# Kernel tuning notes

Measured on AMD Instinct MI355X. Metric: run time of the kernel, lower is better.

## Reference

```python
import jax, jax.numpy as jnp
import numpy as np

NUM_HEADS = 4


def setup_inputs() -> dict:
    key = jax.random.key(0)
    ks = jax.random.split(key, 5)
    B, C, L = 8, 128, 2048
    x = jax.random.normal(ks[0], (B, C, L), dtype=jnp.float32)
    # Conv1d(C, 3C, 1) == per-position linear; weight [3C, C], bias [3C]
    w_qkv = jax.random.normal(ks[1], (3 * C, C), dtype=jnp.float32) * (1.0 / np.sqrt(C))
    b_qkv = jax.random.normal(ks[2], (3 * C,), dtype=jnp.float32) * 0.01
    w_proj = jax.random.normal(ks[3], (C, C), dtype=jnp.float32) * (1.0 / np.sqrt(C))
    b_proj = jax.random.normal(ks[4], (C,), dtype=jnp.float32) * 0.01
    return {"x": x, "w_qkv": w_qkv, "b_qkv": b_qkv, "w_proj": w_proj, "b_proj": b_proj}


def reference(x, w_qkv, b_qkv, w_proj, b_proj):
    B, C, L = x.shape
    H = NUM_HEADS
    D = C // H
    scale = D ** -0.5
    # 1x1 conv qkv projection: [B, 3C, L]
    qkv = jnp.einsum('oc,bcl->bol', w_qkv, x) + b_qkv[None, :, None]
    # reshape (B,3,H,D,L) -> permute to (3,B,H,L,D)
    qkv = qkv.reshape(B, 3, H, D, L).transpose(1, 0, 2, 4, 3)
    q, k, v = qkv[0], qkv[1], qkv[2]  # each [B, H, L, D]
    attn = jax.nn.softmax(jnp.einsum('bhld,bhmd->bhlm', q, k) * scale, axis=-1)
    out = jnp.einsum('bhlm,bhmd->bhld', attn, v)  # [B, H, L, D]
    out = out.transpose(0, 1, 3, 2).reshape(B, C, L)
    out = jnp.einsum('oc,bcl->bol', w_proj, out) + b_proj[None, :, None]
    return out + x
```

## Files before the change

### kernel.cpp

```cpp
#include <hip/hip_runtime.h>

#define Bsz 8
#define Cdim 128
#define Lseq 2048
#define NH 4
#define HD 32
#define BH 32
#define QSCALE (0.17677669529663687f * 1.4426950408889634f)

typedef __bf16 bf16x8 __attribute__((ext_vector_type(8)));
typedef float f32x4 __attribute__((ext_vector_type(4)));
typedef unsigned u32x4 __attribute__((ext_vector_type(4)));

__device__ __forceinline__ float fexp2(float x) {
#if __has_builtin(__builtin_amdgcn_exp2f)
    return __builtin_amdgcn_exp2f(x);
#else
    return __expf(x * 0.6931471805599453f);
#endif
}

__device__ __forceinline__ unsigned short f2bf(float f) {
    unsigned u = __builtin_bit_cast(unsigned, f);
    u += 0x7FFFu + ((u >> 16) & 1u);
    return (unsigned short)(u >> 16);
}

__device__ __forceinline__ unsigned pack_bf16(float a, float b) {
    return (unsigned)f2bf(a) | ((unsigned)f2bf(b) << 16);
}

__device__ __forceinline__ unsigned pack_bf16_rtz(float a, float b) {
    return __builtin_amdgcn_perm(__builtin_bit_cast(unsigned, b),
                                 __builtin_bit_cast(unsigned, a), 0x07060302u);
}

__device__ __forceinline__ float bf_lo(unsigned u) {
    return __builtin_bit_cast(float, u << 16);
}
__device__ __forceinline__ float bf_hi(unsigned u) {
    return __builtin_bit_cast(float, u & 0xFFFF0000u);
}

#define MFMA16(A, B, C) __builtin_amdgcn_mfma_f32_16x16x32_bf16((A), (B), (C), 0, 0, 0)

__global__ __launch_bounds__(256) void qkv_kernel(const float* __restrict__ x,
        const float* __restrict__ w, const float* __restrict__ bias,
        unsigned short* __restrict__ qh, unsigned short* __restrict__ kh,
        unsigned short* __restrict__ vh) {
    __shared__ __attribute__((aligned(16))) unsigned short T[64][132];
    int bid = blockIdx.x;
    int xcd = bid & 7;
    int s   = bid >> 3;
    int og3 = s % 3;
    int u_  = s / 3;
    int trio = u_ * 8 + xcd;
    int lt  = trio & 31;
    int b   = trio >> 5;
    int l0 = lt * 64;
    int t = threadIdx.x;
    int lane = t & 63, wv = t >> 6;
    int m16 = lane & 15, quad = lane >> 4;

    bf16x8 af[2][4];
    float bs[2][4];
    #pragma unroll
    for (int os = 0; os < 2; os++) {
        int orow = og3 * 128 + os * 64 + wv * 16;
        #pragma unroll
        for (int ks = 0; ks < 4; ks++) {
            const float* p = w + (size_t)(orow + m16) * Cdim + ks * 32 + quad * 8;
            float4 f0 = *(const float4*)p;
            float4 f1 = *(const float4*)(p + 4);
            u32x4 u = {pack_bf16(f0.x, f0.y), pack_bf16(f0.z, f0.w),
                       pack_bf16(f1.x, f1.y), pack_bf16(f1.z, f1.w)};
            af[os][ks] = __builtin_bit_cast(bf16x8, u);
        }
        #pragma unroll
        for (int r = 0; r < 4; r++) bs[os][r] = bias[orow + quad * 4 + r];
    }

    {
        int ll = t & 63, cg = t >> 6;
        const float* xb = x + (size_t)b * Cdim * Lseq + l0 + ll;
        #pragma unroll
        for (int i = 0; i < 16; i++) {
            int c = cg * 32 + 2 * i;
            float f0 = xb[(size_t)c * Lseq];
            float f1 = xb[(size_t)(c + 1) * Lseq];
            *(unsigned*)&T[ll][c] = pack_bf16(f0, f1);
        }
    }
    __syncthreads();

    #pragma unroll
    for (int ns = 0; ns < 4; ns++) {
        bf16x8 bx[4];
        #pragma unroll
        for (int ks = 0; ks < 4; ks++)
            bx[ks] = *(const bf16x8*)(&T[ns * 16 + m16][ks * 32 + quad * 8]);
        int l = l0 + ns * 16 + m16;
        #pragma unroll
        for (int os = 0; os < 2; os++) {
            f32x4 acc = {0.f, 0.f, 0.f, 0.f};
            #pragma unroll
            for (int ks = 0; ks < 4; ks++) acc = MFMA16(af[os][ks], bx[ks], acc);
            int oq = os * 64 + wv * 16 + quad * 4;
            if (og3 == 0) {
                int h = oq >> 5, d0 = oq & 31;
                uint2 u;
                u.x = pack_bf16((acc[0] + bs[os][0]) * QSCALE, (acc[1] + bs[os][1]) * QSCALE);
                u.y = pack_bf16((acc[2] + bs[os][2]) * QSCALE, (acc[3] + bs[os][3]) * QSCALE);
                *(uint2*)(qh + ((size_t)(b * NH + h) * Lseq + l) * HD + d0) = u;
            } else if (og3 == 1) {
                int h = oq >> 5, d0 = oq & 31;
                uint2 u;
                u.x = pack_bf16(acc[0] + bs[os][0], acc[1] + bs[os][1]);
                u.y = pack_bf16(acc[2] + bs[os][2], acc[3] + bs[os][3]);
                *(uint2*)(kh + ((size_t)(b * NH + h) * Lseq + l) * HD + d0) = u;
            } else {
                int kc = l >> 6, kk = l & 63;
                int half = kk >> 5, k32 = kk & 31;
                int q_, j_;
                if (k32 < 16) { q_ = k32 >> 2; j_ = k32 & 3; }
                else          { q_ = (k32 - 16) >> 2; j_ = 4 + ((k32 - 16) & 3); }
                int pos = half * 32 + q_ * 8 + j_;
                #pragma unroll
                for (int r = 0; r < 4; r++) {
                    int o = oq + r, h = o >> 5, d = o & 31;
                    vh[(((size_t)(b * NH + h) * 32 + kc) * HD + d) * 64 + pos] =
                        f2bf(acc[r] + bs[os][r]);
                }
            }
        }
    }
}

__global__ __launch_bounds__(256, 2) void attn_kernel(
        const unsigned short* __restrict__ qh, const unsigned short* __restrict__ kh,
        const unsigned short* __restrict__ vh, unsigned short* __restrict__ oo) {
    __shared__ __attribute__((aligned(16))) char smem[49152];

    int bid = blockIdx.x;
    int xcd  = bid & 7;
    int rest = bid >> 3;
    int qt = rest & 15;
    int g  = rest >> 4;
    int bh = xcd + 8 * g;

    int lane = threadIdx.x & 63;
    int wv   = threadIdx.x >> 6;
    int m16  = lane & 15;
    int quad = lane >> 4;
    int l0 = qt * 128;

    bf16x8 qf[2][4];
    #pragma unroll
    for (int qt2 = 0; qt2 < 2; qt2++)
        #pragma unroll
        for (int qs = 0; qs < 4; qs++)
            qf[qt2][qs] = *(const bf16x8*)(
                qh + ((size_t)bh * Lseq + l0 + qt2 * 64 + qs * 16 + m16) * HD + quad * 8);

    f32x4 oacc[2][4][2];
    float sacc[2][4];
    #pragma unroll
    for (int qt2 = 0; qt2 < 2; qt2++)
        #pragma unroll
        for (int qs = 0; qs < 4; qs++) {
            oacc[qt2][qs][0] = f32x4{0.f, 0.f, 0.f, 0.f};
            oacc[qt2][qs][1] = f32x4{0.f, 0.f, 0.f, 0.f};
            sacc[qt2][qs]    = 0.f;
        }
    f32x4 zero = {0.f, 0.f, 0.f, 0.f};

    const unsigned short* kb = kh + (size_t)bh * Lseq * HD + m16 * HD + quad * 8;
    const unsigned short* vb = vh + (size_t)bh * 32 * HD * 64;
    int kbase = wv * 512;

    auto load_kv = [&](int chunk, bf16x8* kf, bf16x8* vf) {
        int k0 = kbase + chunk * 64;
        #pragma unroll
        for (int t = 0; t < 4; t++)
            kf[t] = *(const bf16x8*)(kb + (size_t)(k0 + 16 * t) * HD);
        const unsigned short* vch = vb + (size_t)(k0 >> 6) * (HD * 64);
        vf[0] = *(const bf16x8*)(vch + m16 * 64 + quad * 8);
        vf[1] = *(const bf16x8*)(vch + (16 + m16) * 64 + quad * 8);
        vf[2] = *(const bf16x8*)(vch + m16 * 64 + 32 + quad * 8);
        vf[3] = *(const bf16x8*)(vch + (16 + m16) * 64 + 32 + quad * 8);
    };

    auto compute = [&](const bf16x8* kf, const bf16x8* vf) {
        #pragma unroll
        for (int qt2 = 0; qt2 < 2; qt2++) {
            #pragma unroll
            for (int qs = 0; qs < 4; qs++) {
                f32x4 s0 = MFMA16(kf[0], qf[qt2][qs], zero);
                f32x4 s1 = MFMA16(kf[1], qf[qt2][qs], zero);
                f32x4 s2 = MFMA16(kf[2], qf[qt2][qs], zero);
                f32x4 s3 = MFMA16(kf[3], qf[qt2][qs], zero);
                float p00 = fexp2(s0[0]), p01 = fexp2(s0[1]), p02 = fexp2(s0[2]), p03 = fexp2(s0[3]);
                float p10 = fexp2(s1[0]), p11 = fexp2(s1[1]), p12 = fexp2(s1[2]), p13 = fexp2(s1[3]);
                float p20 = fexp2(s2[0]), p21 = fexp2(s2[1]), p22 = fexp2(s2[2]), p23 = fexp2(s2[3]);
                float p30 = fexp2(s3[0]), p31 = fexp2(s3[1]), p32 = fexp2(s3[2]), p33 = fexp2(s3[3]);
                float r0 = (p00 + p01) + (p02 + p03);
                float r1 = (p10 + p11) + (p12 + p13);
                float r2 = (p20 + p21) + (p22 + p23);
                float r3 = (p30 + p31) + (p32 + p33);
                sacc[qt2][qs] += (r0 + r1) + (r2 + r3);
                u32x4 lo = {pack_bf16_rtz(p00, p01), pack_bf16_rtz(p02, p03),
                            pack_bf16_rtz(p10, p11), pack_bf16_rtz(p12, p13)};
                u32x4 hi = {pack_bf16_rtz(p20, p21), pack_bf16_rtz(p22, p23),
                            pack_bf16_rtz(p30, p31), pack_bf16_rtz(p32, p33)};
                bf16x8 pfL = __builtin_bit_cast(bf16x8, lo);
                bf16x8 pfH = __builtin_bit_cast(bf16x8, hi);
                oacc[qt2][qs][0] = MFMA16(vf[0], pfL, oacc[qt2][qs][0]);
                oacc[qt2][qs][1] = MFMA16(vf[1], pfL, oacc[qt2][qs][1]);
                oacc[qt2][qs][0] = MFMA16(vf[2], pfH, oacc[qt2][qs][0]);
                oacc[qt2][qs][1] = MFMA16(vf[3], pfH, oacc[qt2][qs][1]);
            }
        }
    };

    bf16x8 kA[4], vA[4], kB[4], vB[4];
    load_kv(0, kA, vA);
    load_kv(1, kB, vB);
    compute(kA, vA); load_kv(2, kA, vA);
    compute(kB, vB); load_kv(3, kB, vB);
    compute(kA, vA); load_kv(4, kA, vA);
    compute(kB, vB); load_kv(5, kB, vB);
    compute(kA, vA); load_kv(6, kA, vA);
    compute(kB, vB); load_kv(7, kB, vB);
    compute(kA, vA);
    compute(kB, vB);

    unsigned* red_o = (unsigned*)smem;
    float* red_l = (float*)(smem + 40960);
    #pragma unroll
    for (int qt2 = 0; qt2 < 2; qt2++)
        #pragma unroll
        for (int qs = 0; qs < 4; qs++) {
            int row = qt2 * 64 + qs * 16 + m16;
            unsigned* rw = red_o + (size_t)(wv * 128 + row) * 20;
            *(uint2*)(rw + 2 * quad) =
                make_uint2(pack_bf16_rtz(oacc[qt2][qs][0][0], oacc[qt2][qs][0][1]),
                           pack_bf16_rtz(oacc[qt2][qs][0][2], oacc[qt2][qs][0][3]));
            *(uint2*)(rw + 8 + 2 * quad) =
                make_uint2(pack_bf16_rtz(oacc[qt2][qs][1][0], oacc[qt2][qs][1][1]),
                           pack_bf16_rtz(oacc[qt2][qs][1][2], oacc[qt2][qs][1][3]));
            red_l[(wv * 128 + row) * 4 + quad] = sacc[qt2][qs];
        }
    __syncthreads();

    int q = threadIdx.x >> 1;
    int hcol = threadIdx.x & 1;
    int s8 = hcol * 8;
    float a16[16];
    #pragma unroll
    for (int i = 0; i < 16; i++) a16[i] = 0.f;
    float ltot = 0.f;
    #pragma unroll
    for (int w = 0; w < 4; w++) {
        const unsigned* rr = red_o + (size_t)(w * 128 + q) * 20 + s8;
        uint4 ua = *(const uint4*)rr;
        uint4 ub = *(const uint4*)(rr + 4);
        a16[0]  += bf_lo(ua.x); a16[1]  += bf_hi(ua.x);
        a16[2]  += bf_lo(ua.y); a16[3]  += bf_hi(ua.y);
        a16[4]  += bf_lo(ua.z); a16[5]  += bf_hi(ua.z);
        a16[6]  += bf_lo(ua.w); a16[7]  += bf_hi(ua.w);
        a16[8]  += bf_lo(ub.x); a16[9]  += bf_hi(ub.x);
        a16[10] += bf_lo(ub.y); a16[11] += bf_hi(ub.y);
        a16[12] += bf_lo(ub.z); a16[13] += bf_hi(ub.z);
        a16[14] += bf_lo(ub.w); a16[15] += bf_hi(ub.w);
        float4 lv = *(const float4*)(red_l + (size_t)(w * 128 + q) * 4);
        ltot += (lv.x + lv.y) + (lv.z + lv.w);
    }
    float inv = 1.0f / ltot;
    uint4 u0, u1;
    u0.x = pack_bf16(a16[0] * inv,  a16[1] * inv);
    u0.y = pack_bf16(a16[2] * inv,  a16[3] * inv);
    u0.z = pack_bf16(a16[4] * inv,  a16[5] * inv);
    u0.w = pack_bf16(a16[6] * inv,  a16[7] * inv);
    u1.x = pack_bf16(a16[8] * inv,  a16[9] * inv);
    u1.y = pack_bf16(a16[10] * inv, a16[11] * inv);
    u1.z = pack_bf16(a16[12] * inv, a16[13] * inv);
    u1.w = pack_bf16(a16[14] * inv, a16[15] * inv);
    unsigned short* op = oo + ((size_t)bh * Lseq + l0 + q) * HD + hcol * 16;
    *(uint4*)op = u0;
    *(uint4*)(op + 8) = u1;
}

__global__ __launch_bounds__(256) void proj_kernel(const float* __restrict__ wp,
        const unsigned short* __restrict__ oo, const float* __restrict__ bias,
        const float* __restrict__ x, float* __restrict__ out) {
    int bid = blockIdx.x;
    int ot = bid & 1;
    int nt = bid >> 1;
    int n0 = nt * 32;
    int t = threadIdx.x;
    int lane = t & 63;
    int wv = t >> 6;
    int m16 = lane & 15, quad = lane >> 4;
    int o0 = ot * 64 + wv * 16;

    bf16x8 af[4];
    #pragma unroll
    for (int ks = 0; ks < 4; ks++) {
        const float* p = wp + (size_t)(o0 + m16) * Cdim + ks * 32 + quad * 8;
        float4 f0 = *(const float4*)p;
        float4 f1 = *(const float4*)(p + 4);
        u32x4 u = {pack_bf16(f0.x, f0.y), pack_bf16(f0.z, f0.w),
                   pack_bf16(f1.x, f1.y), pack_bf16(f1.z, f1.w)};
        af[ks] = __builtin_bit_cast(bf16x8, u);
    }
    float bs[4];
    #pragma unroll
    for (int r = 0; r < 4; r++) bs[r] = bias[o0 + quad * 4 + r];
    int oq = o0 + quad * 4;

    #pragma unroll
    for (int lt2 = 0; lt2 < 2; lt2++) {
        int n = n0 + lt2 * 16 + m16;
        int b = n >> 11, l = n & (Lseq - 1);
        bf16x8 bx[4];
        #pragma unroll
        for (int ks = 0; ks < 4; ks++)
            bx[ks] = *(const bf16x8*)(oo + ((size_t)(b * NH + ks) * Lseq + l) * HD + quad * 8);
        f32x4 acc = {0.f, 0.f, 0.f, 0.f};
        #pragma unroll
        for (int ks = 0; ks < 4; ks++) acc = MFMA16(af[ks], bx[ks], acc);
        #pragma unroll
        for (int r = 0; r < 4; r++) {
            size_t xi = ((size_t)b * Cdim + oq + r) * Lseq + l;
            out[xi] = acc[r] + bs[r] + x[xi];
        }
    }
}

extern "C" void kernel_launch(void* const* d_in, const int* in_sizes, int n_in,
                              void* d_out, int out_size, void* d_ws, size_t ws_size,
                              hipStream_t stream) {
    const float* x      = (const float*)d_in[0];
    const float* w_qkv  = (const float*)d_in[1];
    const float* b_qkv  = (const float*)d_in[2];
    const float* w_proj = (const float*)d_in[3];
    const float* b_proj = (const float*)d_in[4];
    float* out = (float*)d_out;

    const size_t E = (size_t)BH * Lseq * HD;
    unsigned short* qh = (unsigned short*)d_ws;
    unsigned short* kh = qh + E;
    unsigned short* vh = kh + E;
    unsigned short* oo = vh + E;

    qkv_kernel<<<dim3(768), dim3(256), 0, stream>>>(x, w_qkv, b_qkv, qh, kh, vh);
    attn_kernel<<<dim3(512), dim3(256), 0, stream>>>(qh, kh, vh, oo);
    proj_kernel<<<dim3(1024), dim3(256), 0, stream>>>(w_proj, oo, b_proj, x, out);
}
```

Before: 108.6 us.

## Stage V in LDS for coalesced stores, add MFMA priority and triple-buffer KV

The QKV kernel now writes the V tile into a shared-memory buffer and then emits 16-byte coalesced stores in the permuted V layout, replacing scattered 2-byte global stores. The attention kernel raises wave priority around MFMA groups with s_setprio and deepens the K/V register prefetch from two buffers to three. The extra LDS tile and the additional register buffers increase resource pressure and may lower occupancy or cause spills.

```diff
diff --git a/kernel.cpp b/kernel.cpp
--- a/kernel.cpp
+++ b/kernel.cpp
@@ -49,6 +49,7 @@
         unsigned short* __restrict__ qh, unsigned short* __restrict__ kh,
         unsigned short* __restrict__ vh) {
     __shared__ __attribute__((aligned(16))) unsigned short T[64][132];
+    __shared__ __attribute__((aligned(16))) unsigned short V2[64][132];
     int bid = blockIdx.x;
     int xcd = bid & 7;
     int s   = bid >> 3;
@@ -119,19 +120,36 @@
                 u.y = pack_bf16(acc[2] + bs[os][2], acc[3] + bs[os][3]);
                 *(uint2*)(kh + ((size_t)(b * NH + h) * Lseq + l) * HD + d0) = u;
             } else {
-                int kc = l >> 6, kk = l & 63;
-                int half = kk >> 5, k32 = kk & 31;
-                int q_, j_;
-                if (k32 < 16) { q_ = k32 >> 2; j_ = k32 & 3; }
-                else          { q_ = (k32 - 16) >> 2; j_ = 4 + ((k32 - 16) & 3); }
-                int pos = half * 32 + q_ * 8 + j_;
-                #pragma unroll
-                for (int r = 0; r < 4; r++) {
-                    int o = oq + r, h = o >> 5, d = o & 31;
-                    vh[(((size_t)(b * NH + h) * 32 + kc) * HD + d) * 64 + pos] =
-                        f2bf(acc[r] + bs[os][r]);
-                }
+                int kk = l & 63;
+                uint2 u;
+                u.x = pack_bf16(acc[0] + bs[os][0], acc[1] + bs[os][1]);
+                u.y = pack_bf16(acc[2] + bs[os][2], acc[3] + bs[os][3]);
+                *(uint2*)&V2[kk][oq] = u;
             }
+        }
+    }
+
+    if (og3 == 2) {
+        __syncthreads();
+        int kc = l0 >> 6;
+        #pragma unroll
+        for (int s2 = 0; s2 < 4; s2++) {
+            int i = t + 256 * s2;
+            int o = i >> 3;
+            int pos0 = (i & 7) * 8;
+            int half = pos0 >> 5, qq = (pos0 & 31) >> 3;
+            int kb2 = half * 32 + qq * 4;
+            unsigned short e0 = V2[kb2 + 0][o], e1 = V2[kb2 + 1][o];
+            unsigned short e2 = V2[kb2 + 2][o], e3 = V2[kb2 + 3][o];
+            unsigned short e4 = V2[kb2 + 16][o], e5 = V2[kb2 + 17][o];
+            unsigned short e6 = V2[kb2 + 18][o], e7 = V2[kb2 + 19][o];
+            uint4 u;
+            u.x = (unsigned)e0 | ((unsigned)e1 << 16);
+            u.y = (unsigned)e2 | ((unsigned)e3 << 16);
+            u.z = (unsigned)e4 | ((unsigned)e5 << 16);
+            u.w = (unsigned)e6 | ((unsigned)e7 << 16);
+            int h = o >> 5, d = o & 31;
+            *(uint4*)(vh + (((size_t)(b * NH + h) * 32 + kc) * HD + d) * 64 + pos0) = u;
         }
     }
 }
@@ -195,10 +213,12 @@
         for (int qt2 = 0; qt2 < 2; qt2++) {
             #pragma unroll
             for (int qs = 0; qs < 4; qs++) {
+                __builtin_amdgcn_s_setprio(1);
                 f32x4 s0 = MFMA16(kf[0], qf[qt2][qs], zero);
                 f32x4 s1 = MFMA16(kf[1], qf[qt2][qs], zero);
                 f32x4 s2 = MFMA16(kf[2], qf[qt2][qs], zero);
                 f32x4 s3 = MFMA16(kf[3], qf[qt2][qs], zero);
+                __builtin_amdgcn_s_setprio(0);
                 float p00 = fexp2(s0[0]), p01 = fexp2(s0[1]), p02 = fexp2(s0[2]), p03 = fexp2(s0[3]);
                 float p10 = fexp2(s1[0]), p11 = fexp2(s1[1]), p12 = fexp2(s1[2]), p13 = fexp2(s1[3]);
                 float p20 = fexp2(s2[0]), p21 = fexp2(s2[1]), p22 = fexp2(s2[2]), p23 = fexp2(s2[3]);
@@ -214,23 +234,26 @@
                             pack_bf16_rtz(p30, p31), pack_bf16_rtz(p32, p33)};
                 bf16x8 pfL = __builtin_bit_cast(bf16x8, lo);
                 bf16x8 pfH = __builtin_bit_cast(bf16x8, hi);
+                __builtin_amdgcn_s_setprio(1);
                 oacc[qt2][qs][0] = MFMA16(vf[0], pfL, oacc[qt2][qs][0]);
                 oacc[qt2][qs][1] = MFMA16(vf[1], pfL, oacc[qt2][qs][1]);
                 oacc[qt2][qs][0] = MFMA16(vf[2], pfH, oacc[qt2][qs][0]);
                 oacc[qt2][qs][1] = MFMA16(vf[3], pfH, oacc[qt2][qs][1]);
+                __builtin_amdgcn_s_setprio(0);
             }
         }
     };
 
-    bf16x8 kA[4], vA[4], kB[4], vB[4];
+    bf16x8 kA[4], vA[4], kB[4], vB[4], kC[4], vC[4];
     load_kv(0, kA, vA);
     load_kv(1, kB, vB);
-    compute(kA, vA); load_kv(2, kA, vA);
-    compute(kB, vB); load_kv(3, kB, vB);
-    compute(kA, vA); load_kv(4, kA, vA);
-    compute(kB, vB); load_kv(5, kB, vB);
+    load_kv(2, kC, vC);
+    compute(kA, vA); load_kv(3, kA, vA);
+    compute(kB, vB); load_kv(4, kB, vB);
+    compute(kC, vC); load_kv(5, kC, vC);
     compute(kA, vA); load_kv(6, kA, vA);
     compute(kB, vB); load_kv(7, kB, vB);
+    compute(kC, vC);
     compute(kA, vA);
     compute(kB, vB);
 
```

New measurement: 110.1 us. No clear change (+1.4%).
